# Performance work log

Hardware: AMD Instinct MI355X
Metric: run time of the kernel (lower is better)

Reference implementation:

```python
import jax, jax.numpy as jnp
import numpy as np

K_NEIGHBORS = 20


def setup_inputs() -> dict:
    key = jax.random.key(0)
    ks = jax.random.split(key, 13)
    B, C, N = 8, 3, 4096
    s = lambda k_, shape, fan: jax.random.normal(k_, shape, jnp.float32) * (1.0 / np.sqrt(fan))
    return {
        "x": jax.random.normal(ks[0], (B, C, N), jnp.float32),
        "W1": s(ks[1], (64, 6), 6),      "b1": jnp.zeros((64,), jnp.float32),
        "W2": s(ks[2], (128, 64), 64),   "b2": jnp.zeros((128,), jnp.float32),
        "Wi": s(ks[3], (1024, 128), 128),"bi": jnp.zeros((1024,), jnp.float32),
        "Wg1": s(ks[4], (512, 1024), 1024), "bg1": jnp.zeros((512,), jnp.float32),
        "Wg2": s(ks[5], (256, 512), 512),   "bg2": jnp.zeros((256,), jnp.float32),
        "Wl": s(ks[6], (9, 256), 256),      "bl": jnp.zeros((9,), jnp.float32),
    }


def _tnet(x, W1, b1, W2, b2, Wi, bi, Wg1, bg1, Wg2, bg2, Wl, bl):
    B, C, N = x.shape
    # pairwise squared distance: ||xi||^2 - 2 xi.xj + ||xj||^2  -> (B, N, N)
    inner = jnp.einsum("bcn,bcm->bnm", x, x)
    sq = jnp.sum(x * x, axis=1)  # (B, N)
    dist = sq[:, :, None] - 2.0 * inner + sq[:, None, :]
    # k nearest neighbours (smallest distance)
    _, knn = jax.lax.top_k(-dist, K_NEIGHBORS)  # (B, N, k)
    # gather neighbour features directly (no (B,C,N,N) tile)
    central = x[:, :, :, None]                                   # (B, C, N, 1)
    neigh = jnp.take_along_axis(x[:, :, None, :], knn[:, None, :, :], axis=-1)  # (B, C, N, k)
    edge = jnp.concatenate(
        [jnp.broadcast_to(central, neigh.shape), neigh - central], axis=1
    )  # (B, 2C, N, k)
    # local 1x1 conv2d blocks (conv + relu)
    h = jax.nn.relu(jnp.einsum("oc,bcnk->bonk", W1, edge) + b1[None, :, None, None])
    h = jax.nn.relu(jnp.einsum("oc,bcnk->bonk", W2, h) + b2[None, :, None, None])
    h = jnp.max(h, axis=-1)  # max over k -> (B, 128, N)
    # inter 1x1 conv1d block
    h = jax.nn.relu(jnp.einsum("oc,bcn->bon", Wi, h) + bi[None, :, None])
    g = jnp.max(h, axis=-1)  # global max over nodes -> (B, 1024)
    # global MLP
    g = jax.nn.relu(g @ Wg1.T + bg1)
    g = jax.nn.relu(g @ Wg2.T + bg2)
    out = g @ Wl.T + bl  # (B, 9)
    out = out.reshape(B, 3, 3) + jnp.eye(3, dtype=out.dtype)
    return out


def reference(x, W1, b1, W2, b2, Wi, bi, Wg1, bg1, Wg2, bg2, Wl, bl):
    return _tnet(x, W1, b1, W2, b2, Wi, bi, Wg1, bg1, Wg2, bg2, Wl, bl)
```

## Files before the change

kernel.cpp:

```cpp
#include <hip/hip_runtime.h>
#include <stdint.h>

typedef unsigned long long u64;
typedef unsigned short ushort_t;
#define NPTS 4096
#define KNN 20

using bf16x8 = __attribute__((ext_vector_type(8))) short;
using f32x4  = __attribute__((ext_vector_type(4))) float;
using f32x2  = __attribute__((ext_vector_type(2))) float;

__device__ __forceinline__ unsigned orderbits(float f) {
  unsigned u = __float_as_uint(f);
  return ((int)u < 0) ? ~u : (u | 0x80000000u);
}

__device__ __forceinline__ ushort_t f2bf(float f) {
  unsigned u = __float_as_uint(f);
  u += 0x7fffu + ((u >> 16) & 1u);
  return (ushort_t)(u >> 16);
}

__device__ __forceinline__ u64 shflxor64(u64 v, int m) {
  unsigned lo = __shfl_xor((unsigned)(v & 0xffffffffull), m, 64);
  unsigned hi = __shfl_xor((unsigned)(v >> 32), m, 64);
  return (((u64)hi) << 32) | lo;
}

__device__ __forceinline__ float dist_exact(float4 q, float4 a) {
  float inner = __fadd_rn(__fadd_rn(__fmul_rn(q.x, a.x), __fmul_rn(q.y, a.y)),
                          __fmul_rn(q.z, a.z));
  return __fadd_rn(__fsub_rn(q.w, __fmul_rn(2.0f, inner)), a.w);
}

__device__ __forceinline__ f32x2 dist2(f32x2 qx, f32x2 qy, f32x2 qz, f32x2 qw,
                                       float4 a) {
#pragma clang fp contract(off)
  f32x2 ax = {a.x, a.x}, ay = {a.y, a.y}, az = {a.z, a.z}, aw = {a.w, a.w};
  f32x2 t0 = qx * ax;
  f32x2 t1 = qy * ay;
  f32x2 t2 = qz * az;
  f32x2 inner = (t0 + t1) + t2;
  f32x2 two = {2.0f, 2.0f};
  return (qw - two * inner) + aw;
}

__device__ __forceinline__ unsigned bucket_of(float d) {
  unsigned bits = __float_as_uint(fmaxf(d, 0.f));
  int t = (int)(bits >> 18) - 3680;
  return (unsigned)min(max(t, 0), 1023);
}

__global__ __launch_bounds__(256) void prep_kernel(const float* __restrict__ x,
                                                   float4* __restrict__ xT4) {
  int i = blockIdx.x * 256 + threadIdx.x;
  int b = i >> 12, m = i & 4095;
  const float* xb = x + (size_t)b * 3 * NPTS;
  float a0 = xb[m], a1 = xb[NPTS + m], a2 = xb[2 * NPTS + m];
  float sq = __fadd_rn(__fadd_rn(__fmul_rn(a0, a0), __fmul_rn(a1, a1)),
                       __fmul_rn(a2, a2));
  xT4[i] = make_float4(a0, a1, a2, sq);
}

#define NB 1024
#define PPB 4
#define CCAP 128
__global__ __launch_bounds__(256) void knn_kernel(const float4* __restrict__ xT4,
                                                  int* __restrict__ knn_out) {
  __shared__ unsigned hist[PPB * NB];
  __shared__ u64 cand[PPB * CCAP];
  __shared__ unsigned sB[PPB], sCnt[PPB], sCand[PPB];

  const int tid = threadIdx.x;
  const int bid = blockIdx.x;
  const int b = bid >> 10;
  const int n0 = (bid & 1023) * PPB;
  const float4* xb4 = xT4 + (size_t)b * NPTS;

  float4 q[PPB];
#pragma unroll
  for (int p = 0; p < PPB; ++p) q[p] = xb4[n0 + p];
  const f32x2 qx01 = {q[0].x, q[1].x}, qy01 = {q[0].y, q[1].y},
              qz01 = {q[0].z, q[1].z}, qw01 = {q[0].w, q[1].w};
  const f32x2 qx23 = {q[2].x, q[3].x}, qy23 = {q[2].y, q[3].y},
              qz23 = {q[2].z, q[3].z}, qw23 = {q[2].w, q[3].w};

  for (int i = tid; i < PPB * NB; i += 256) hist[i] = 0;
  if (tid < PPB) { sCnt[tid] = 0; sCand[tid] = 0; }
  __syncthreads();

  unsigned kL[16], kH[16];
#pragma unroll 4
  for (int it = 0; it < 16; ++it) {
    const int m = it * 256 + tid;
    float4 a = xb4[m];
    f32x2 d01 = dist2(qx01, qy01, qz01, qw01, a);
    f32x2 d23 = dist2(qx23, qy23, qz23, qw23, a);
    unsigned bk0 = bucket_of(d01[0]);
    unsigned bk1 = bucket_of(d01[1]);
    unsigned bk2 = bucket_of(d23[0]);
    unsigned bk3 = bucket_of(d23[1]);
    atomicAdd(&hist[0 * NB + bk0], 1u);
    atomicAdd(&hist[1 * NB + bk1], 1u);
    atomicAdd(&hist[2 * NB + bk2], 1u);
    atomicAdd(&hist[3 * NB + bk3], 1u);
    kL[it] = bk0 | (bk1 << 16);
    kH[it] = bk2 | (bk3 << 16);
  }
  __syncthreads();

  const int lane = tid & 63, wv = tid >> 6;
  {
    unsigned h[16]; unsigned local = 0;
    const int hb = wv * NB + lane * 16;
#pragma unroll
    for (int j = 0; j < 16; ++j) { h[j] = hist[hb + j]; local += h[j]; }
    unsigned incl = local;
    for (int off = 1; off < 64; off <<= 1) {
      unsigned v = __shfl_up(incl, off, 64);
      if (lane >= off) incl += v;
    }
    unsigned excl = incl - local;
    if (excl < KNN && incl >= KNN) {
      unsigned cum = excl;
#pragma unroll
      for (int j = 0; j < 16; ++j) {
        if (cum + h[j] >= KNN) { sB[wv] = lane * 16 + j; break; }
        cum += h[j];
      }
    }
  }
  __syncthreads();

  const unsigned B0 = sB[0], B1 = sB[1], B2 = sB[2], B3 = sB[3];
  for (int it = 0; it < 16; ++it) {
    const int m = it * 256 + tid;
    unsigned ks[PPB];
    ks[0] = kL[it] & 0xffffu; ks[1] = kL[it] >> 16;
    ks[2] = kH[it] & 0xffffu; ks[3] = kH[it] >> 16;
    unsigned Bs[PPB] = {B0, B1, B2, B3};
#pragma unroll
    for (int p = 0; p < PPB; ++p) {
      if (ks[p] < Bs[p]) {
        unsigned s = atomicAdd(&sCnt[p], 1u);
        knn_out[((size_t)((b << 12) + n0 + p)) * KNN + s] = m;
      } else if (ks[p] == Bs[p]) {
        float d = dist_exact(q[p], xb4[m]);
        unsigned s = atomicAdd(&sCand[p], 1u);
        if (s < CCAP) cand[p * CCAP + s] = (((u64)orderbits(d)) << 32) | (unsigned)m;
      }
    }
  }
  __syncthreads();

  {
    const int nsel = (int)sCnt[wv];
    const int ncand = min((int)sCand[wv], CCAP);
    const int ntake = KNN - nsel;
    const size_t base = ((size_t)((b << 12) + n0 + wv)) * KNN;
    volatile u64* vc = &cand[wv * CCAP];
    for (int t = 0; t < ntake; ++t) {
      u64 mk = ~0ull;
      for (int i = lane; i < ncand; i += 64) { u64 v = vc[i]; if (v < mk) mk = v; }
      for (int off = 32; off; off >>= 1) { u64 o = shflxor64(mk, off); if (o < mk) mk = o; }
      if (lane == 0) knn_out[base + nsel + t] = (int)(unsigned)(mk & 0xffffffffull);
      for (int i = lane; i < ncand; i += 64) { if (vc[i] == mk) vc[i] = ~0ull; }
    }
  }
}

__global__ __launch_bounds__(256, 2) void edge_fused(
    const float4* __restrict__ xT4, const int* __restrict__ knn,
    const float* __restrict__ W1, const float* __restrict__ b1,
    const ushort_t* __restrict__ w2B, const float* __restrict__ b2,
    ushort_t* __restrict__ hT) {
  __shared__ __align__(16) ushort_t h1S[8 * 32 * 64];
  __shared__ __align__(16) ushort_t w2S[128 * 64];
  const int tid = threadIdx.x;
  const int lane = tid & 63, wv = tid >> 6;
  const int ln = lane & 15, quad = lane >> 4;

  {
    const int4* wg = (const int4*)w2B;
#pragma unroll
    for (int j = 0; j < 4; ++j) {
      int q = j * 256 + tid;
      int row = q >> 3, c = q & 7;
      ((int4*)w2S)[row * 8 + (c ^ (row & 7))] = wg[q];
    }
  }
  float b2r[8];
#pragma unroll
  for (int n = 0; n < 8; ++n) b2r[n] = b2[n * 16 + ln];

  {
    const int p = tid >> 5, s5 = tid & 31;
    const int idx = blockIdx.x * 8 + p;
    const int b = idx >> 12, n = idx & 4095;
    const float4* xb4 = xT4 + ((size_t)b << 12);
    const float4 c4 = xb4[n];
    const int c0 = 2 * s5;
    float w1a[6], w1b[6];
#pragma unroll
    for (int j = 0; j < 6; ++j) {
      w1a[j] = W1[c0 * 6 + j];
      w1b[j] = W1[(c0 + 1) * 6 + j];
    }
    const float b1a = b1[c0], b1b = b1[c0 + 1];
    const int kbase = idx * KNN;
    unsigned* h1d = (unsigned*)h1S;
#pragma unroll 4
    for (int k = 0; k < KNN; ++k) {
      int nb = knn[kbase + k];
      float4 a4 = xb4[nb];
      float e3 = a4.x - c4.x, e4 = a4.y - c4.y, e5 = a4.z - c4.z;
      float za = b1a, zb = b1b;
      za = fmaf(w1a[0], c4.x, za); zb = fmaf(w1b[0], c4.x, zb);
      za = fmaf(w1a[1], c4.y, za); zb = fmaf(w1b[1], c4.y, zb);
      za = fmaf(w1a[2], c4.z, za); zb = fmaf(w1b[2], c4.z, zb);
      za = fmaf(w1a[3], e3, za);   zb = fmaf(w1b[3], e3, zb);
      za = fmaf(w1a[4], e4, za);   zb = fmaf(w1b[4], e4, zb);
      za = fmaf(w1a[5], e5, za);   zb = fmaf(w1b[5], e5, zb);
      unsigned pk = (unsigned)f2bf(fmaxf(za, 0.f)) |
                    ((unsigned)f2bf(fmaxf(zb, 0.f)) << 16);
      int row = p * 32 + k;
      int dw = row * 32 + (((s5 >> 2) ^ (row & 7)) << 2) + (s5 & 3);
      h1d[dw] = pk;
    }
  }
  __syncthreads();

  bf16x8 Bf[8][2];
#pragma unroll
  for (int n = 0; n < 8; ++n)
#pragma unroll
    for (int s = 0; s < 2; ++s) {
      int row = n * 16 + ln;
      Bf[n][s] = *(const bf16x8*)&w2S[row * 64 + (((s * 4 + quad) ^ (ln & 7)) << 3)];
    }

  const int base_idx = blockIdx.x * 8;
#pragma unroll
  for (int pi = 0; pi < 2; ++pi) {
    const int ps = wv * 2 + pi;
    const int sw = ln & 7;
    float vmax[8];
    {
      const int row = ps * 32 + ln;
      bf16x8 A0 = *(const bf16x8*)&h1S[row * 64 + (((0 + quad) ^ sw) << 3)];
      bf16x8 A1 = *(const bf16x8*)&h1S[row * 64 + (((4 + quad) ^ sw) << 3)];
      f32x4 acc;
#pragma unroll
      for (int n = 0; n < 8; ++n) {
        acc = (f32x4){0.f, 0.f, 0.f, 0.f};
        acc = __builtin_amdgcn_mfma_f32_16x16x32_bf16(A0, Bf[n][0], acc, 0, 0, 0);
        acc = __builtin_amdgcn_mfma_f32_16x16x32_bf16(A1, Bf[n][1], acc, 0, 0, 0);
        vmax[n] = fmaxf(fmaxf(acc[0], acc[1]), fmaxf(acc[2], acc[3]));
      }
    }
    {
      const int row = ps * 32 + 16 + ln;
      bf16x8 A0 = *(const bf16x8*)&h1S[row * 64 + (((0 + quad) ^ sw) << 3)];
      bf16x8 A1 = *(const bf16x8*)&h1S[row * 64 + (((4 + quad) ^ sw) << 3)];
      f32x4 acc;
#pragma unroll
      for (int n = 0; n < 8; ++n) {
        acc = (f32x4){0.f, 0.f, 0.f, 0.f};
        acc = __builtin_amdgcn_mfma_f32_16x16x32_bf16(A0, Bf[n][0], acc, 0, 0, 0);
        acc = __builtin_amdgcn_mfma_f32_16x16x32_bf16(A1, Bf[n][1], acc, 0, 0, 0);
        float v1 = (quad == 0)
                       ? fmaxf(fmaxf(acc[0], acc[1]), fmaxf(acc[2], acc[3]))
                       : -INFINITY;
        vmax[n] = fmaxf(vmax[n], v1);
      }
    }
    const int gidx = base_idx + ps;
#pragma unroll
    for (int n = 0; n < 8; ++n) {
      float v = vmax[n];
      v = fmaxf(v, __shfl_xor(v, 16, 64));
      v = fmaxf(v, __shfl_xor(v, 32, 64));
      if (quad == 0) {
        hT[(size_t)gidx * 128 + n * 16 + ln] = f2bf(fmaxf(v + b2r[n], 0.f));
      }
    }
  }
}

__global__ __launch_bounds__(256) void convert_weights(
    const float* __restrict__ Wi, const float* __restrict__ W2,
    ushort_t* __restrict__ wiB, ushort_t* __restrict__ w2B) {
  int i = blockIdx.x * 256 + threadIdx.x;
  if (i < 131072) wiB[i] = f2bf(Wi[i]);
  if (i < 8192)   w2B[i] = f2bf(W2[i]);
}

#define LDP 136
__global__ __launch_bounds__(256, 2) void inception_mfma(
    const ushort_t* __restrict__ hT, const ushort_t* __restrict__ wiB,
    const float* __restrict__ bi, unsigned* __restrict__ g) {
  __shared__ __align__(16) ushort_t hS[128 * LDP];
  __shared__ __align__(16) ushort_t wS[128 * LDP];
  const int tid = threadIdx.x;
  const int b = blockIdx.z;
  const int m0 = blockIdx.x * 128;
  const int n0 = blockIdx.y * 128;

  const ushort_t* hg = hT + ((size_t)b * NPTS + m0) * 128;
  const ushort_t* wg = wiB + (size_t)n0 * 128;
#pragma unroll
  for (int i = 0; i < 8; ++i) {
    int chunk = i * 256 + tid;
    int row = chunk >> 4, c = chunk & 15;
    *(int4*)&hS[row * LDP + c * 8] = *(const int4*)&hg[row * 128 + c * 8];
    *(int4*)&wS[row * LDP + c * 8] = *(const int4*)&wg[row * 128 + c * 8];
  }
  __syncthreads();

  const int lane = tid & 63, wid = tid >> 6;
  const int ln = lane & 15, quad = lane >> 4;
  const int mw = (wid >> 1) * 64, nw = (wid & 1) * 64;

  f32x4 acc[4][4];
#pragma unroll
  for (int mi = 0; mi < 4; ++mi)
#pragma unroll
    for (int ni = 0; ni < 4; ++ni) acc[mi][ni] = (f32x4){0.f, 0.f, 0.f, 0.f};

#pragma unroll
  for (int kk = 0; kk < 4; ++kk) {
    bf16x8 af[4], bfr[4];
    const int ko = kk * 32 + quad * 8;
#pragma unroll
    for (int mi = 0; mi < 4; ++mi)
      af[mi] = *(const bf16x8*)&hS[(mw + mi * 16 + ln) * LDP + ko];
#pragma unroll
    for (int ni = 0; ni < 4; ++ni)
      bfr[ni] = *(const bf16x8*)&wS[(nw + ni * 16 + ln) * LDP + ko];
#pragma unroll
    for (int mi = 0; mi < 4; ++mi)
#pragma unroll
      for (int ni = 0; ni < 4; ++ni)
        acc[mi][ni] = __builtin_amdgcn_mfma_f32_16x16x32_bf16(
            af[mi], bfr[ni], acc[mi][ni], 0, 0, 0);
  }

#pragma unroll
  for (int ni = 0; ni < 4; ++ni) {
    float v = acc[0][ni][0];
#pragma unroll
    for (int mi = 0; mi < 4; ++mi)
#pragma unroll
      for (int r = 0; r < 4; ++r) v = fmaxf(v, acc[mi][ni][r]);
    v = fmaxf(v, __shfl_xor(v, 16, 64));
    v = fmaxf(v, __shfl_xor(v, 32, 64));
    if (quad == 0) {
      int o = n0 + nw + ni * 16 + ln;
      float val = fmaxf(v + bi[o], 0.f);
      atomicMax(&g[b * 1024 + o], __float_as_uint(val));
    }
  }
}

__global__ __launch_bounds__(512) void head_kernel(
    const unsigned* __restrict__ g, const float* __restrict__ Wg1,
    const float* __restrict__ bg1, const float* __restrict__ Wg2,
    const float* __restrict__ bg2, const float* __restrict__ Wl,
    const float* __restrict__ bl, float* __restrict__ out) {
  __shared__ __align__(16) float gl[1024];
  __shared__ __align__(16) float g1l[512];
  __shared__ __align__(16) float g2l[256];
  const int tid = threadIdx.x;
  const int b = blockIdx.x;
  for (int i = tid; i < 1024; i += 512) gl[i] = __uint_as_float(g[b * 1024 + i]);
  __syncthreads();
  {
    const float4* w = (const float4*)(Wg1 + (size_t)tid * 1024);
    const float4* gv = (const float4*)gl;
    float a0 = bg1[tid], a1 = 0.f, a2 = 0.f, a3 = 0.f;
    for (int j = 0; j < 256; j += 4) {
      float4 w0 = w[j], w1 = w[j+1], w2 = w[j+2], w3 = w[j+3];
      float4 v0 = gv[j], v1 = gv[j+1], v2 = gv[j+2], v3 = gv[j+3];
      a0 = fmaf(w0.x, v0.x, a0); a0 = fmaf(w0.y, v0.y, a0);
      a0 = fmaf(w0.z, v0.z, a0); a0 = fmaf(w0.w, v0.w, a0);
      a1 = fmaf(w1.x, v1.x, a1); a1 = fmaf(w1.y, v1.y, a1);
      a1 = fmaf(w1.z, v1.z, a1); a1 = fmaf(w1.w, v1.w, a1);
      a2 = fmaf(w2.x, v2.x, a2); a2 = fmaf(w2.y, v2.y, a2);
      a2 = fmaf(w2.z, v2.z, a2); a2 = fmaf(w2.w, v2.w, a2);
      a3 = fmaf(w3.x, v3.x, a3); a3 = fmaf(w3.y, v3.y, a3);
      a3 = fmaf(w3.z, v3.z, a3); a3 = fmaf(w3.w, v3.w, a3);
    }
    g1l[tid] = fmaxf((a0 + a1) + (a2 + a3), 0.f);
  }
  __syncthreads();
  if (tid < 256) {
    const float4* w = (const float4*)(Wg2 + (size_t)tid * 512);
    const float4* gv = (const float4*)g1l;
    float a0 = bg2[tid], a1 = 0.f;
    for (int j = 0; j < 128; j += 2) {
      float4 w0 = w[j], w1 = w[j+1];
      float4 v0 = gv[j], v1 = gv[j+1];
      a0 = fmaf(w0.x, v0.x, a0); a0 = fmaf(w0.y, v0.y, a0);
      a0 = fmaf(w0.z, v0.z, a0); a0 = fmaf(w0.w, v0.w, a0);
      a1 = fmaf(w1.x, v1.x, a1); a1 = fmaf(w1.y, v1.y, a1);
      a1 = fmaf(w1.z, v1.z, a1); a1 = fmaf(w1.w, v1.w, a1);
    }
    g2l[tid] = fmaxf(a0 + a1, 0.f);
  }
  __syncthreads();
  if (tid < 9) {
    float acc = bl[tid];
    for (int c = 0; c < 256; ++c) acc = fmaf(Wl[tid * 256 + c], g2l[c], acc);
    if (tid == 0 || tid == 4 || tid == 8) acc += 1.0f;
    out[b * 9 + tid] = acc;
  }
}

extern "C" void kernel_launch(void* const* d_in, const int* in_sizes, int n_in,
                              void* d_out, int out_size, void* d_ws, size_t ws_size,
                              hipStream_t stream) {
  const float* x   = (const float*)d_in[0];
  const float* W1  = (const float*)d_in[1];
  const float* b1  = (const float*)d_in[2];
  const float* W2  = (const float*)d_in[3];
  const float* b2  = (const float*)d_in[4];
  const float* Wi  = (const float*)d_in[5];
  const float* bi  = (const float*)d_in[6];
  const float* Wg1 = (const float*)d_in[7];
  const float* bg1 = (const float*)d_in[8];
  const float* Wg2 = (const float*)d_in[9];
  const float* bg2 = (const float*)d_in[10];
  const float* Wl  = (const float*)d_in[11];
  const float* bl  = (const float*)d_in[12];

  int*       knn = (int*)d_ws;
  ushort_t*  hT  = (ushort_t*)((char*)d_ws + (3u << 20));
  ushort_t*  wiB = (ushort_t*)((char*)d_ws + (12u << 20));
  ushort_t*  w2B = (ushort_t*)((char*)d_ws + (12u << 20) + (512u << 10));
  float4*    xT4 = (float4*)((char*)d_ws + (13u << 20));
  unsigned*  g   = (unsigned*)((char*)d_ws + (14u << 20));

  prep_kernel<<<128, 256, 0, stream>>>(x, xT4);
  knn_kernel<<<8 * NPTS / PPB, 256, 0, stream>>>(xT4, knn);
  convert_weights<<<512, 256, 0, stream>>>(Wi, W2, wiB, w2B);
  edge_fused<<<8 * NPTS / 8, 256, 0, stream>>>(xT4, knn, W1, b1, w2B, b2, hT);
  hipMemsetAsync(g, 0, 8 * 1024 * sizeof(unsigned), stream);
  inception_mfma<<<dim3(32, 8, 8), 256, 0, stream>>>(hT, wiB, bi, g);
  head_kernel<<<8, 512, 0, stream>>>(g, Wg1, bg1, Wg2, bg2, Wl, bl, (float*)d_out);
}
```

Before: 327.7 us.

## Merge setup kernels, coarsen kNN histogram, shrink edge blocks, split head GEMV

Folds the point transpose, the bf16 weight conversion and the zeroing of the global-max buffer into one setup kernel, which removes two launches and a memset. The kNN distance histogram drops from 1024 to 512 buckets so the prefix scan is cheaper, at the cost of more candidates landing in the boundary bucket. edge_fused now handles 4 points per block instead of 8, and half the threads stage W2 while the other half build h1, aiming for higher occupancy. The serial 8-block head kernel is split so the large Wg1 GEMV runs over 64 blocks.

```diff
diff --git a/kernel.cpp b/kernel.cpp
--- a/kernel.cpp
+++ b/kernel.cpp
@@ -47,22 +47,29 @@
 
 __device__ __forceinline__ unsigned bucket_of(float d) {
   unsigned bits = __float_as_uint(fmaxf(d, 0.f));
-  int t = (int)(bits >> 18) - 3680;
-  return (unsigned)min(max(t, 0), 1023);
-}
-
-__global__ __launch_bounds__(256) void prep_kernel(const float* __restrict__ x,
-                                                   float4* __restrict__ xT4) {
+  int t = (int)(bits >> 19) - 1840;
+  return (unsigned)min(max(t, 0), 511);
+}
+
+__global__ __launch_bounds__(256) void setup_kernel(
+    const float* __restrict__ x, const float* __restrict__ Wi,
+    const float* __restrict__ W2, float4* __restrict__ xT4,
+    ushort_t* __restrict__ wiB, ushort_t* __restrict__ w2B,
+    unsigned* __restrict__ g) {
   int i = blockIdx.x * 256 + threadIdx.x;
-  int b = i >> 12, m = i & 4095;
-  const float* xb = x + (size_t)b * 3 * NPTS;
-  float a0 = xb[m], a1 = xb[NPTS + m], a2 = xb[2 * NPTS + m];
-  float sq = __fadd_rn(__fadd_rn(__fmul_rn(a0, a0), __fmul_rn(a1, a1)),
-                       __fmul_rn(a2, a2));
-  xT4[i] = make_float4(a0, a1, a2, sq);
-}
-
-#define NB 1024
+  wiB[i] = f2bf(Wi[i]);
+  if (i < 32768) {
+    int b = i >> 12, m = i & 4095;
+    const float* xb = x + (size_t)b * 3 * NPTS;
+    float a0 = xb[m], a1 = xb[NPTS + m], a2 = xb[2 * NPTS + m];
+    float sq = __fadd_rn(__fadd_rn(__fmul_rn(a0, a0), __fmul_rn(a1, a1)),
+                         __fmul_rn(a2, a2));
+    xT4[i] = make_float4(a0, a1, a2, sq);
+  }
+  if (i < 8192) { w2B[i] = f2bf(W2[i]); g[i] = 0u; }
+}
+
+#define NB 512
 #define PPB 4
 #define CCAP 128
 __global__ __launch_bounds__(256) void knn_kernel(const float4* __restrict__ xT4,
@@ -111,10 +118,10 @@
 
   const int lane = tid & 63, wv = tid >> 6;
   {
-    unsigned h[16]; unsigned local = 0;
-    const int hb = wv * NB + lane * 16;
-#pragma unroll
-    for (int j = 0; j < 16; ++j) { h[j] = hist[hb + j]; local += h[j]; }
+    unsigned h[8]; unsigned local = 0;
+    const int hb = wv * NB + lane * 8;
+#pragma unroll
+    for (int j = 0; j < 8; ++j) { h[j] = hist[hb + j]; local += h[j]; }
     unsigned incl = local;
     for (int off = 1; off < 64; off <<= 1) {
       unsigned v = __shfl_up(incl, off, 64);
@@ -124,8 +131,8 @@
     if (excl < KNN && incl >= KNN) {
       unsigned cum = excl;
 #pragma unroll
-      for (int j = 0; j < 16; ++j) {
-        if (cum + h[j] >= KNN) { sB[wv] = lane * 16 + j; break; }
+      for (int j = 0; j < 8; ++j) {
+        if (cum + h[j] >= KNN) { sB[wv] = lane * 8 + j; break; }
         cum += h[j];
       }
     }
@@ -169,33 +176,20 @@
   }
 }
 
-__global__ __launch_bounds__(256, 2) void edge_fused(
+__global__ __launch_bounds__(256, 4) void edge_fused(
     const float4* __restrict__ xT4, const int* __restrict__ knn,
     const float* __restrict__ W1, const float* __restrict__ b1,
     const ushort_t* __restrict__ w2B, const float* __restrict__ b2,
     ushort_t* __restrict__ hT) {
-  __shared__ __align__(16) ushort_t h1S[8 * 32 * 64];
+  __shared__ __align__(16) ushort_t h1S[4 * 32 * 64];
   __shared__ __align__(16) ushort_t w2S[128 * 64];
   const int tid = threadIdx.x;
   const int lane = tid & 63, wv = tid >> 6;
   const int ln = lane & 15, quad = lane >> 4;
 
-  {
-    const int4* wg = (const int4*)w2B;
-#pragma unroll
-    for (int j = 0; j < 4; ++j) {
-      int q = j * 256 + tid;
-      int row = q >> 3, c = q & 7;
-      ((int4*)w2S)[row * 8 + (c ^ (row & 7))] = wg[q];
-    }
-  }
-  float b2r[8];
-#pragma unroll
-  for (int n = 0; n < 8; ++n) b2r[n] = b2[n * 16 + ln];
-
-  {
+  if (tid < 128) {
     const int p = tid >> 5, s5 = tid & 31;
-    const int idx = blockIdx.x * 8 + p;
+    const int idx = blockIdx.x * 4 + p;
     const int b = idx >> 12, n = idx & 4095;
     const float4* xb4 = xT4 + ((size_t)b << 12);
     const float4 c4 = xb4[n];
@@ -227,7 +221,19 @@
       int dw = row * 32 + (((s5 >> 2) ^ (row & 7)) << 2) + (s5 & 3);
       h1d[dw] = pk;
     }
-  }
+  } else {
+    const int t = tid - 128;
+    const int4* wg = (const int4*)w2B;
+#pragma unroll
+    for (int j = 0; j < 8; ++j) {
+      int qq = j * 128 + t;
+      int row = qq >> 3, c = qq & 7;
+      ((int4*)w2S)[row * 8 + (c ^ (row & 7))] = wg[qq];
+    }
+  }
+  float b2r[8];
+#pragma unroll
+  for (int n = 0; n < 8; ++n) b2r[n] = b2[n * 16 + ln];
   __syncthreads();
 
   bf16x8 Bf[8][2];
@@ -239,60 +245,48 @@
       Bf[n][s] = *(const bf16x8*)&w2S[row * 64 + (((s * 4 + quad) ^ (ln & 7)) << 3)];
     }
 
-  const int base_idx = blockIdx.x * 8;
-#pragma unroll
-  for (int pi = 0; pi < 2; ++pi) {
-    const int ps = wv * 2 + pi;
-    const int sw = ln & 7;
-    float vmax[8];
-    {
-      const int row = ps * 32 + ln;
-      bf16x8 A0 = *(const bf16x8*)&h1S[row * 64 + (((0 + quad) ^ sw) << 3)];
-      bf16x8 A1 = *(const bf16x8*)&h1S[row * 64 + (((4 + quad) ^ sw) << 3)];
-      f32x4 acc;
-#pragma unroll
-      for (int n = 0; n < 8; ++n) {
-        acc = (f32x4){0.f, 0.f, 0.f, 0.f};
-        acc = __builtin_amdgcn_mfma_f32_16x16x32_bf16(A0, Bf[n][0], acc, 0, 0, 0);
-        acc = __builtin_amdgcn_mfma_f32_16x16x32_bf16(A1, Bf[n][1], acc, 0, 0, 0);
-        vmax[n] = fmaxf(fmaxf(acc[0], acc[1]), fmaxf(acc[2], acc[3]));
-      }
-    }
-    {
-      const int row = ps * 32 + 16 + ln;
-      bf16x8 A0 = *(const bf16x8*)&h1S[row * 64 + (((0 + quad) ^ sw) << 3)];
-      bf16x8 A1 = *(const bf16x8*)&h1S[row * 64 + (((4 + quad) ^ sw) << 3)];
-      f32x4 acc;
-#pragma unroll
-      for (int n = 0; n < 8; ++n) {
-        acc = (f32x4){0.f, 0.f, 0.f, 0.f};
-        acc = __builtin_amdgcn_mfma_f32_16x16x32_bf16(A0, Bf[n][0], acc, 0, 0, 0);
-        acc = __builtin_amdgcn_mfma_f32_16x16x32_bf16(A1, Bf[n][1], acc, 0, 0, 0);
-        float v1 = (quad == 0)
-                       ? fmaxf(fmaxf(acc[0], acc[1]), fmaxf(acc[2], acc[3]))
-                       : -INFINITY;
-        vmax[n] = fmaxf(vmax[n], v1);
-      }
-    }
-    const int gidx = base_idx + ps;
+  const int ps = wv;
+  const int sw = ln & 7;
+  float vmax[8];
+  {
+    const int row = ps * 32 + ln;
+    bf16x8 A0 = *(const bf16x8*)&h1S[row * 64 + (((0 + quad) ^ sw) << 3)];
+    bf16x8 A1 = *(const bf16x8*)&h1S[row * 64 + (((4 + quad) ^ sw) << 3)];
+    f32x4 acc;
 #pragma unroll
     for (int n = 0; n < 8; ++n) {
-      float v = vmax[n];
-      v = fmaxf(v, __shfl_xor(v, 16, 64));
-      v = fmaxf(v, __shfl_xor(v, 32, 64));
-      if (quad == 0) {
-        hT[(size_t)gidx * 128 + n * 16 + ln] = f2bf(fmaxf(v + b2r[n], 0.f));
-      }
-    }
-  }
-}
-
-__global__ __launch_bounds__(256) void convert_weights(
-    const float* __restrict__ Wi, const float* __restrict__ W2,
-    ushort_t* __restrict__ wiB, ushort_t* __restrict__ w2B) {
-  int i = blockIdx.x * 256 + threadIdx.x;
-  if (i < 131072) wiB[i] = f2bf(Wi[i]);
-  if (i < 8192)   w2B[i] = f2bf(W2[i]);
+      acc = (f32x4){0.f, 0.f, 0.f, 0.f};
+      acc = __builtin_amdgcn_mfma_f32_16x16x32_bf16(A0, Bf[n][0], acc, 0, 0, 0);
+      acc = __builtin_amdgcn_mfma_f32_16x16x32_bf16(A1, Bf[n][1], acc, 0, 0, 0);
+      vmax[n] = fmaxf(fmaxf(acc[0], acc[1]), fmaxf(acc[2], acc[3]));
+    }
+  }
+  {
+    const int row = ps * 32 + 16 + ln;
+    bf16x8 A0 = *(const bf16x8*)&h1S[row * 64 + (((0 + quad) ^ sw) << 3)];
+    bf16x8 A1 = *(const bf16x8*)&h1S[row * 64 + (((4 + quad) ^ sw) << 3)];
+    f32x4 acc;
+#pragma unroll
+    for (int n = 0; n < 8; ++n) {
+      acc = (f32x4){0.f, 0.f, 0.f, 0.f};
+      acc = __builtin_amdgcn_mfma_f32_16x16x32_bf16(A0, Bf[n][0], acc, 0, 0, 0);
+      acc = __builtin_amdgcn_mfma_f32_16x16x32_bf16(A1, Bf[n][1], acc, 0, 0, 0);
+      float v1 = (quad == 0)
+                     ? fmaxf(fmaxf(acc[0], acc[1]), fmaxf(acc[2], acc[3]))
+                     : -INFINITY;
+      vmax[n] = fmaxf(vmax[n], v1);
+    }
+  }
+  const int gidx = blockIdx.x * 4 + ps;
+#pragma unroll
+  for (int n = 0; n < 8; ++n) {
+    float v = vmax[n];
+    v = fmaxf(v, __shfl_xor(v, 16, 64));
+    v = fmaxf(v, __shfl_xor(v, 32, 64));
+    if (quad == 0) {
+      hT[(size_t)gidx * 128 + n * 16 + ln] = f2bf(fmaxf(v + b2r[n], 0.f));
+    }
+  }
 }
 
 #define LDP 136
@@ -362,38 +356,47 @@
   }
 }
 
-__global__ __launch_bounds__(512) void head_kernel(
+__global__ __launch_bounds__(256) void head1_kernel(
     const unsigned* __restrict__ g, const float* __restrict__ Wg1,
-    const float* __restrict__ bg1, const float* __restrict__ Wg2,
+    const float* __restrict__ bg1, float* __restrict__ g1) {
+  const int b = blockIdx.x >> 3, slice = blockIdx.x & 7;
+  const int tid = threadIdx.x;
+  const int ol = tid >> 2, part = tid & 3;
+  const int o = slice * 64 + ol;
+  const float4* w = (const float4*)(Wg1 + (size_t)o * 1024 + part * 256);
+  const float4* gv = (const float4*)((const float*)(g + b * 1024) + part * 256);
+  float a0 = 0.f, a1 = 0.f, a2 = 0.f, a3 = 0.f;
+#pragma unroll
+  for (int j = 0; j < 64; j += 4) {
+    float4 w0 = w[j], w1 = w[j+1], w2 = w[j+2], w3 = w[j+3];
+    float4 v0 = gv[j], v1 = gv[j+1], v2 = gv[j+2], v3 = gv[j+3];
+    a0 = fmaf(w0.x, v0.x, a0); a0 = fmaf(w0.y, v0.y, a0);
+    a0 = fmaf(w0.z, v0.z, a0); a0 = fmaf(w0.w, v0.w, a0);
+    a1 = fmaf(w1.x, v1.x, a1); a1 = fmaf(w1.y, v1.y, a1);
+    a1 = fmaf(w1.z, v1.z, a1); a1 = fmaf(w1.w, v1.w, a1);
+    a2 = fmaf(w2.x, v2.x, a2); a2 = fmaf(w2.y, v2.y, a2);
+    a2 = fmaf(w2.z, v2.z, a2); a2 = fmaf(w2.w, v2.w, a2);
+    a3 = fmaf(w3.x, v3.x, a3); a3 = fmaf(w3.y, v3.y, a3);
+    a3 = fmaf(w3.z, v3.z, a3); a3 = fmaf(w3.w, v3.w, a3);
+  }
+  float s = (a0 + a1) + (a2 + a3);
+  s += __shfl_xor(s, 1, 64);
+  s += __shfl_xor(s, 2, 64);
+  if (part == 0) g1[b * 512 + o] = fmaxf(s + bg1[o], 0.f);
+}
+
+__global__ __launch_bounds__(256) void head2_kernel(
+    const float* __restrict__ g1, const float* __restrict__ Wg2,
     const float* __restrict__ bg2, const float* __restrict__ Wl,
     const float* __restrict__ bl, float* __restrict__ out) {
-  __shared__ __align__(16) float gl[1024];
   __shared__ __align__(16) float g1l[512];
   __shared__ __align__(16) float g2l[256];
   const int tid = threadIdx.x;
   const int b = blockIdx.x;
-  for (int i = tid; i < 1024; i += 512) gl[i] = __uint_as_float(g[b * 1024 + i]);
+  g1l[tid] = g1[b * 512 + tid];
+  g1l[tid + 256] = g1[b * 512 + 256 + tid];
   __syncthreads();
   {
-    const float4* w = (const float4*)(Wg1 + (size_t)tid * 1024);
-    const float4* gv = (const float4*)gl;
-    float a0 = bg1[tid], a1 = 0.f, a2 = 0.f, a3 = 0.f;
-    for (int j = 0; j < 256; j += 4) {
-      float4 w0 = w[j], w1 = w[j+1], w2 = w[j+2], w3 = w[j+3];
-      float4 v0 = gv[j], v1 = gv[j+1], v2 = gv[j+2], v3 = gv[j+3];
-      a0 = fmaf(w0.x, v0.x, a0); a0 = fmaf(w0.y, v0.y, a0);
-      a0 = fmaf(w0.z, v0.z, a0); a0 = fmaf(w0.w, v0.w, a0);
-      a1 = fmaf(w1.x, v1.x, a1); a1 = fmaf(w1.y, v1.y, a1);
-      a1 = fmaf(w1.z, v1.z, a1); a1 = fmaf(w1.w, v1.w, a1);
-      a2 = fmaf(w2.x, v2.x, a2); a2 = fmaf(w2.y, v2.y, a2);
-      a2 = fmaf(w2.z, v2.z, a2); a2 = fmaf(w2.w, v2.w, a2);
-      a3 = fmaf(w3.x, v3.x, a3); a3 = fmaf(w3.y, v3.y, a3);
-      a3 = fmaf(w3.z, v3.z, a3); a3 = fmaf(w3.w, v3.w, a3);
-    }
-    g1l[tid] = fmaxf((a0 + a1) + (a2 + a3), 0.f);
-  }
-  __syncthreads();
-  if (tid < 256) {
     const float4* w = (const float4*)(Wg2 + (size_t)tid * 512);
     const float4* gv = (const float4*)g1l;
     float a0 = bg2[tid], a1 = 0.f;
@@ -439,12 +442,12 @@
   ushort_t*  w2B = (ushort_t*)((char*)d_ws + (12u << 20) + (512u << 10));
   float4*    xT4 = (float4*)((char*)d_ws + (13u << 20));
   unsigned*  g   = (unsigned*)((char*)d_ws + (14u << 20));
-
-  prep_kernel<<<128, 256, 0, stream>>>(x, xT4);
+  float*     g1  = (float*)((char*)d_ws + (14u << 20) + (64u << 10));
+
+  setup_kernel<<<512, 256, 0, stream>>>(x, Wi, W2, xT4, wiB, w2B, g);
   knn_kernel<<<8 * NPTS / PPB, 256, 0, stream>>>(xT4, knn);
-  convert_weights<<<512, 256, 0, stream>>>(Wi, W2, wiB, w2B);
-  edge_fused<<<8 * NPTS / 8, 256, 0, stream>>>(xT4, knn, W1, b1, w2B, b2, hT);
-  hipMemsetAsync(g, 0, 8 * 1024 * sizeof(unsigned), stream);
+  edge_fused<<<8 * NPTS / 4, 256, 0, stream>>>(xT4, knn, W1, b1, w2B, b2, hT);
   inception_mfma<<<dim3(32, 8, 8), 256, 0, stream>>>(hT, wiB, bi, g);
-  head_kernel<<<8, 512, 0, stream>>>(g, Wg1, bg1, Wg2, bg2, Wl, bl, (float*)d_out);
-}
+  head1_kernel<<<64, 256, 0, stream>>>(g, Wg1, bg1, g1);
+  head2_kernel<<<8, 256, 0, stream>>>(g1, Wg2, bg2, Wl, bl, (float*)d_out);
+}
```

After: 267.3 us (median of 2 runs). 1.23x faster.
